# Optimization experiments

Measured on AMD Instinct MI355X. Metric: run time of the kernel, lower is better.

The kernel has to match this reference:

```python
import jax, jax.numpy as jnp
import numpy as np

N_HEADS = 16
ROPE_THETA = 10000.0


def _rope_cos_sin(T, head_dim, dtype):
    # freqs: (head_dim//2,), angles: (T, head_dim//2)
    freqs = 1.0 / ROPE_THETA ** (jnp.arange(0, head_dim, 2, dtype=jnp.float32) / head_dim)
    ang = jnp.arange(T, dtype=jnp.float32)[:, None] * freqs[None, :]
    return jnp.cos(ang).astype(dtype), jnp.sin(ang).astype(dtype)


def _apply_rope(x, cos, sin):
    # x: (B, H, T, D); cos/sin: (T, D//2)
    D = x.shape[-1]
    x1, x2 = x[..., : D // 2], x[..., D // 2 :]
    return jnp.concatenate([x1 * cos - x2 * sin, x1 * sin + x2 * cos], axis=-1)


def setup_inputs() -> dict:
    key = jax.random.key(0)
    ks = jax.random.split(key, 5)
    B, T, C = 2, 2048, 1024
    x = jax.random.normal(ks[0], (B, T, C), dtype=jnp.float32)
    w_attn = jax.random.normal(ks[1], (C, 3 * C), dtype=jnp.float32) * (C ** -0.5)
    b_attn = jax.random.normal(ks[2], (3 * C,), dtype=jnp.float32) * 0.02
    w_proj = jax.random.normal(ks[3], (C, C), dtype=jnp.float32) * (C ** -0.5)
    b_proj = jax.random.normal(ks[4], (C,), dtype=jnp.float32) * 0.02
    return {
        "x": x,
        "w_attn": w_attn,
        "b_attn": b_attn,
        "w_proj": w_proj,
        "b_proj": b_proj,
        "last_k_no_attend": 0,
        "window_size": 0,
    }


def reference(x, w_attn, b_attn, w_proj, b_proj, last_k_no_attend, window_size):
    B, T, C = x.shape
    H = N_HEADS
    D = C // H
    qkv = x @ w_attn + b_attn  # (B, T, 3C)
    q, k, v = jnp.split(qkv, 3, axis=-1)
    # (B, T, C) -> (B, H, T, D)
    to_heads = lambda t: t.reshape(B, T, H, D).transpose(0, 2, 1, 3)
    q, k, v = to_heads(q), to_heads(k), to_heads(v)
    cos, sin = _rope_cos_sin(T, D, x.dtype)
    q = _apply_rope(q, cos, sin)
    k = _apply_rope(k, cos, sin)
    scale = D ** -0.5
    attn = jnp.einsum("bhqd,bhkd->bhqk", q, k) * scale  # (B, H, T, T)
    causal = jnp.tril(jnp.ones((T, T), dtype=bool))
    attn = jnp.where(causal, attn, -jnp.inf)
    # last_k_no_attend/window_size default to 0 -> the custom-mask branch is
    # skipped (the nonzero branch in the source is ill-defined: it zeroes
    # entire rows producing NaN softmax).
    attn = jax.nn.softmax(attn, axis=-1)
    y = jnp.einsum("bhqk,bhkd->bhqd", attn, v)  # (B, H, T, D)
    y = y.transpose(0, 2, 1, 3).reshape(B, T, C)
    return y @ w_proj + b_proj
```

## Files before the change

kernel.cpp:

```cpp
#include <hip/hip_runtime.h>
#include <hip/hip_bf16.h>

typedef __bf16 bf16_t;
typedef __bf16 bf16x8 __attribute__((ext_vector_type(8)));
typedef float f32x4 __attribute__((ext_vector_type(4)));
typedef float f32x8v __attribute__((ext_vector_type(8)));

#define B_    2
#define T_    2048
#define C_    1024
#define H_    16
#define D_    64
#define M_    4096
#define NQKV_ 3072
#define PLD   72
#define NQT2  16
#define GTILE (128 * 64)
#define SLOTE 16384

static __device__ __forceinline__ float  bf2f(bf16_t x) { return (float)x; }
static __device__ __forceinline__ bf16_t f2bf(float x)  { return (bf16_t)x; }

typedef const __attribute__((address_space(1))) void gas_void;
typedef __attribute__((address_space(3))) void las_void;
static __device__ __forceinline__ void gld16(const void* g, void* l) {
  __builtin_amdgcn_global_load_lds((gas_void*)g, (las_void*)l, 16, 0, 0);
}

__global__ __launch_bounds__(256) void rope_tab_k(float2* __restrict__ tab) {
  int i = blockIdx.x * 256 + threadIdx.x;
  int tpos = i >> 5, d = i & 31;
  float fr = exp2f(-(float)d * (13.287712379549449f / 32.0f));
  float ang = (float)tpos * fr;
  tab[i] = make_float2(cosf(ang), sinf(ang));
}

__global__ __launch_bounds__(256) void f32_to_bf16_k(const float* __restrict__ in,
                                                     bf16_t* __restrict__ out) {
  const int i = (blockIdx.x * 256 + threadIdx.x) * 8;
  f32x8v v = *(const f32x8v*)(in + i);
  bf16x8 h;
#pragma unroll
  for (int j = 0; j < 8; ++j) h[j] = f2bf(v[j]);
  *(bf16x8*)(out + i) = h;
}

__global__ __launch_bounds__(256) void transpose_f32_bf16(const float* __restrict__ in,
                                                          bf16_t* __restrict__ out,
                                                          int R, int Ccols) {
  __shared__ bf16_t tile[32][33];
  int tx = threadIdx.x & 31, ty = threadIdx.x >> 5;
  int c0 = blockIdx.x * 32, r0 = blockIdx.y * 32;
#pragma unroll
  for (int j = 0; j < 4; ++j)
    tile[ty + j * 8][tx] = f2bf(in[(size_t)(r0 + ty + j * 8) * Ccols + c0 + tx]);
  __syncthreads();
#pragma unroll
  for (int j = 0; j < 4; ++j)
    out[(size_t)(c0 + ty + j * 8) * R + r0 + tx] = tile[tx][ty + j * 8];
}

__device__ __forceinline__ void gemm_core(const bf16_t* __restrict__ A,
                                          const bf16_t* __restrict__ Bt,
                                          int m0, int n0,
                                          bf16_t* sm,
                                          f32x4 acc[4][4]) {
  const int t    = threadIdx.x;
  const int lane = t & 63, w = t >> 6;
  const int wr = (w >> 1) * 64, wc = (w & 1) * 64;
  const int l15 = lane & 15, g4 = lane >> 4;

  const f32x4 z4 = {0.f, 0.f, 0.f, 0.f};
#pragma unroll
  for (int i = 0; i < 4; ++i)
#pragma unroll
    for (int j = 0; j < 4; ++j) acc[i][j] = z4;

  const int srow = w * 32 + (lane >> 3);
  const int sel8 = (lane & 7) * 8;
  const bf16_t* gA = A  + (size_t)(m0 + srow) * C_ + sel8;
  const bf16_t* gB = Bt + (size_t)(n0 + srow) * C_ + sel8;
  const int dOff = (w * 32) * 64;

#pragma unroll
  for (int j = 0; j < 4; ++j) {
    gld16(gA + (size_t)(j * 8) * C_, sm + dOff + j * 8 * 64);
    gld16(gB + (size_t)(j * 8) * C_, sm + GTILE + dOff + j * 8 * 64);
  }
  __syncthreads();

  int cur = 0;
  for (int kt = 0; kt < C_ / 64; ++kt) {
    if (kt + 1 < C_ / 64) {
      const int k0 = (kt + 1) * 64;
      bf16_t* nA = sm + (cur ^ 1) * (2 * GTILE);
      bf16_t* nB = nA + GTILE;
#pragma unroll
      for (int j = 0; j < 4; ++j) {
        gld16(gA + (size_t)(j * 8) * C_ + k0, nA + dOff + j * 8 * 64);
        gld16(gB + (size_t)(j * 8) * C_ + k0, nB + dOff + j * 8 * 64);
      }
    }
    const bf16_t* lA = sm + cur * (2 * GTILE);
    const bf16_t* lB = lA + GTILE;
#pragma unroll
    for (int ks = 0; ks < 2; ++ks) {
      bf16x8 af[4], bfv[4];
#pragma unroll
      for (int mi = 0; mi < 4; ++mi)
        af[mi] = *(const bf16x8*)&lA[(wr + mi * 16 + l15) * 64 + ks * 32 + g4 * 8];
#pragma unroll
      for (int ni = 0; ni < 4; ++ni)
        bfv[ni] = *(const bf16x8*)&lB[(wc + ni * 16 + l15) * 64 + ks * 32 + g4 * 8];
#pragma unroll
      for (int mi = 0; mi < 4; ++mi)
#pragma unroll
        for (int ni = 0; ni < 4; ++ni)
          acc[mi][ni] = __builtin_amdgcn_mfma_f32_16x16x32_bf16(af[mi], bfv[ni],
                                                                acc[mi][ni], 0, 0, 0);
    }
    __syncthreads();
    cur ^= 1;
  }
}

__global__ __launch_bounds__(512, 2) void qkv_gemm(const bf16_t* __restrict__ x,
                                                   const bf16_t* __restrict__ wT,
                                                   const float* __restrict__ bias,
                                                   const float2* __restrict__ rtab,
                                                   bf16_t* __restrict__ qo,
                                                   bf16_t* __restrict__ ko,
                                                   bf16_t* __restrict__ vo) {
  __shared__ __align__(16) bf16_t sm[4 * SLOTE];
  const int t = threadIdx.x;
  const int lane = t & 63, w = t >> 6;
  const int l15 = lane & 15, g4 = lane >> 4;
  const int wr = (w >> 2) * 128, wc = (w & 3) * 64;

  const int bid = blockIdx.x;
  const int swz = (bid & 7) * 24 + (bid >> 3);
  const int m0 = (swz & 15) * 256, n0 = (swz >> 4) * 256;

  const f32x4 z4 = {0.f, 0.f, 0.f, 0.f};
  f32x4 acc[8][4];
#pragma unroll
  for (int i = 0; i < 8; ++i)
#pragma unroll
    for (int j = 0; j < 4; ++j) acc[i][j] = z4;

  const int sr  = (lane >> 2);
  const int sc8 = (lane & 3) * 8;
  const bf16_t* gA = x  + (size_t)(m0 + w * 32 + sr) * C_ + sc8;
  const bf16_t* gB = wT + (size_t)(n0 + w * 32 + sr) * C_ + sc8;

#define QKV_STAGE(h)                                                            \
  {                                                                             \
    bf16_t* sl = sm + ((h) & 3) * SLOTE;                                        \
    const size_t kofs = (size_t)(h) * 32;                                       \
    gld16(gA + kofs,            sl + (w * 32) * 32);                            \
    gld16(gA + 16 * C_ + kofs,  sl + (w * 32 + 16) * 32);                       \
    gld16(gB + kofs,            sl + 8192 + (w * 32) * 32);                     \
    gld16(gB + 16 * C_ + kofs,  sl + 8192 + (w * 32 + 16) * 32);                \
  }

  QKV_STAGE(0);
  QKV_STAGE(1);

  for (int h = 0; h < 32; ++h) {
    if (h < 31) asm volatile("s_waitcnt vmcnt(4)" ::: "memory");
    else        asm volatile("s_waitcnt vmcnt(0)" ::: "memory");
    __builtin_amdgcn_sched_barrier(0);
    __builtin_amdgcn_s_barrier();
    __builtin_amdgcn_sched_barrier(0);
    if (h + 2 < 32) QKV_STAGE(h + 2);

    const bf16_t* sl = sm + (h & 3) * SLOTE;
    bf16x8 af[8], bfv[4];
#pragma unroll
    for (int mi = 0; mi < 8; ++mi)
      af[mi] = *(const bf16x8*)&sl[(wr + mi * 16 + l15) * 32 + g4 * 8];
#pragma unroll
    for (int ni = 0; ni < 4; ++ni)
      bfv[ni] = *(const bf16x8*)&sl[8192 + (wc + ni * 16 + l15) * 32 + g4 * 8];
#pragma unroll
    for (int mi = 0; mi < 8; ++mi)
#pragma unroll
      for (int ni = 0; ni < 4; ++ni)
        acc[mi][ni] = __builtin_amdgcn_mfma_f32_16x16x32_bf16(af[mi], bfv[ni],
                                                              acc[mi][ni], 0, 0, 0);
  }
#undef QKV_STAGE

  __syncthreads();
  bf16_t* stg = sm + w * 8192;

  const int ng  = n0 + wc;
  const int sel = ng >> 10;
  const int h2  = (ng & 1023) >> 6;

  if (sel < 2) {
    const float qs = (sel == 0) ? 0.125f * 1.4426950408889634f : 1.0f;
#pragma unroll
    for (int mi = 0; mi < 8; ++mi) {
#pragma unroll
      for (int ni = 0; ni < 2; ++ni) {
        const int d1 = ni * 16 + l15;
        const float b1 = bias[ng + d1];
        const float b2 = bias[ng + d1 + 32];
#pragma unroll
        for (int r = 0; r < 4; ++r) {
          const int lrow = mi * 16 + g4 * 4 + r;
          const int tpos = (m0 + wr + lrow) & (T_ - 1);
          const float2 cs = rtab[tpos * 32 + d1];
          const float x1 = acc[mi][ni][r]     + b1;
          const float x2 = acc[mi][ni + 2][r] + b2;
          stg[lrow * 64 + d1]      = f2bf((x1 * cs.x - x2 * cs.y) * qs);
          stg[lrow * 64 + d1 + 32] = f2bf((x1 * cs.y + x2 * cs.x) * qs);
        }
      }
    }
  } else {
#pragma unroll
    for (int mi = 0; mi < 8; ++mi)
#pragma unroll
      for (int ni = 0; ni < 4; ++ni) {
        const int d = ni * 16 + l15;
        const float b1 = bias[ng + d];
#pragma unroll
        for (int r = 0; r < 4; ++r)
          stg[(mi * 16 + g4 * 4 + r) * 64 + d] = f2bf(acc[mi][ni][r] + b1);
      }
  }

  bf16_t* outp = (sel == 0) ? qo : (sel == 1 ? ko : vo);
  const int a  = lane >> 3;
  const int b8 = (lane & 7) * 8;
#pragma unroll
  for (int p = 0; p < 16; ++p) {
    const int lrow = p * 8 + a;
    const int row  = m0 + wr + lrow;
    const int tpos = row & (T_ - 1);
    const int bb   = row >> 11;
    uint4 val = *(const uint4*)&stg[lrow * 64 + b8];
    *(uint4*)(outp + ((size_t)(bb * H_ + h2) * T_ + tpos) * D_ + b8) = val;
  }
}

__global__ __launch_bounds__(512) void attn_fwd(const bf16_t* __restrict__ q,
                                                const bf16_t* __restrict__ k,
                                                const bf16_t* __restrict__ v,
                                                bf16_t* __restrict__ y) {
  __shared__ __align__(16) bf16_t Ks[64 * 64];
  __shared__ __align__(16) bf16_t Vt[64 * PLD];
  const int t = threadIdx.x;
  const int lane = t & 63, w = t >> 6;
  const int l15 = lane & 15, g4 = lane >> 4;

  const int f   = blockIdx.x;
  const int idx = f & 255;
  const int bh  = idx & 31;
  const int p   = idx >> 5;
  const int qt  = (f >> 8) ? (15 - p) : p;
  const int qb  = qt * 128;
  const size_t hb = (size_t)bh * T_ * D_;

  const int qrow = qb + w * 16 + l15;
  bf16x8 qf[2];
  qf[0] = *(const bf16x8*)(q + hb + (size_t)qrow * D_ + g4 * 8);
  qf[1] = *(const bf16x8*)(q + hb + (size_t)qrow * D_ + 32 + g4 * 8);

  const f32x4 z4 = {0.f, 0.f, 0.f, 0.f};
  f32x4 o[4];
#pragma unroll
  for (int i = 0; i < 4; ++i) o[i] = z4;
  float mx = -1e30f, L = 0.f;

  const int skk = t >> 3;
  const int sd0 = (t & 7) * 8;
  const int u   = t & 7;
  const int ksw = sd0 ^ ((skk & 7) * 8);
  const int slot = ((skk >> 5) & 1) * 32 + ((skk >> 2) & 3) * 8 + ((skk >> 4) & 1) * 4 + (skk & 3);
  const int pos  = (((slot >> 3) ^ u) << 3) | (slot & 7);
  const int rowb = qb + w * 16 + g4 * 4;

  const int ntiles = 2 * qt + 2;

  uint4 kv = *(const uint4*)(k + hb + (size_t)skk * D_ + sd0);
  uint4 vv = *(const uint4*)(v + hb + (size_t)skk * D_ + sd0);

  for (int it = 0; it < ntiles; ++it) {
    const int kb = it * 64;
    __syncthreads();
    *(uint4*)&Ks[skk * 64 + ksw] = kv;
    {
      const bf16_t* vb = (const bf16_t*)&vv;
#pragma unroll
      for (int i = 0; i < 8; ++i)
        Vt[(sd0 + i) * PLD + pos] = vb[i];
    }
    __syncthreads();

    if (it + 1 < ntiles) {
      const size_t nb = hb + (size_t)(kb + 64 + skk) * D_ + sd0;
      kv = *(const uint4*)(k + nb);
      vv = *(const uint4*)(v + nb);
    }

    const bool last = (it == ntiles - 1);
    if (last && w < 4) continue;

    f32x4 s[4];
#pragma unroll
    for (int c = 0; c < 4; ++c) s[c] = z4;
#pragma unroll
    for (int ks = 0; ks < 2; ++ks)
#pragma unroll
      for (int c = 0; c < 4; ++c) {
        const int kr = c * 16 + l15;
        bf16x8 kf = *(const bf16x8*)&Ks[kr * 64 + ((ks * 32 + g4 * 8) ^ ((kr & 7) * 8))];
        s[c] = __builtin_amdgcn_mfma_f32_16x16x32_bf16(kf, qf[ks], s[c], 0, 0, 0);
      }

    if (last || (it == ntiles - 2 && w < 4)) {
#pragma unroll
      for (int c = 0; c < 4; ++c)
#pragma unroll
        for (int r = 0; r < 4; ++r)
          if (kb + c * 16 + g4 * 4 + r > qrow) s[c][r] = -1e30f;
    }

    float tm = -1e30f;
#pragma unroll
    for (int c = 0; c < 4; ++c)
#pragma unroll
      for (int r = 0; r < 4; ++r) tm = fmaxf(tm, s[c][r]);
    tm = fmaxf(tm, __shfl_xor(tm, 16));
    tm = fmaxf(tm, __shfl_xor(tm, 32));
    if (!__all(tm - mx <= 8.0f)) {
      const float mnew = fmaxf(mx, tm);
      const float sc = exp2f(mx - mnew);
      L *= sc;
      float scr[4];
#pragma unroll
      for (int r = 0; r < 4; ++r)
        scr[r] = __shfl(sc, (lane & 48) | (g4 * 4 + r));
#pragma unroll
      for (int nf = 0; nf < 4; ++nf)
#pragma unroll
        for (int r = 0; r < 4; ++r) o[nf][r] *= scr[r];
      mx = mnew;
    }
    float rs = 0.f;
#pragma unroll
    for (int c = 0; c < 4; ++c)
#pragma unroll
      for (int r = 0; r < 4; ++r) {
        s[c][r] = exp2f(s[c][r] - mx);
        rs += s[c][r];
      }
    rs += __shfl_xor(rs, 16);
    rs += __shfl_xor(rs, 32);
    L += rs;

    bf16x8 ap0, ap1;
#pragma unroll
    for (int r = 0; r < 4; ++r) {
      ap0[r]     = f2bf(s[0][r]);
      ap0[4 + r] = f2bf(s[1][r]);
      ap1[r]     = f2bf(s[2][r]);
      ap1[4 + r] = f2bf(s[3][r]);
    }

#pragma unroll
    for (int nf = 0; nf < 4; ++nf) {
      const int d  = nf * 16 + l15;
      const int h3 = (2 * nf + (l15 >> 3)) & 7;
      bf16x8 vf0 = *(const bf16x8*)&Vt[d * PLD + ((g4 ^ h3) << 3)];
      bf16x8 vf1 = *(const bf16x8*)&Vt[d * PLD + (((g4 + 4) ^ h3) << 3)];
      o[nf] = __builtin_amdgcn_mfma_f32_16x16x32_bf16(ap0, vf0, o[nf], 0, 0, 0);
      o[nf] = __builtin_amdgcn_mfma_f32_16x16x32_bf16(ap1, vf1, o[nf], 0, 0, 0);
    }
  }

  const int bb = bh / H_, hh = bh % H_;
  float il[4];
#pragma unroll
  for (int r = 0; r < 4; ++r)
    il[r] = 1.0f / __shfl(L, (lane & 48) | (g4 * 4 + r));
#pragma unroll
  for (int nf = 0; nf < 4; ++nf)
#pragma unroll
    for (int r = 0; r < 4; ++r) {
      const int row = rowb + r;
      y[(size_t)(bb * T_ + row) * C_ + hh * D_ + nf * 16 + l15] = f2bf(o[nf][r] * il[r]);
    }
}

__global__ __launch_bounds__(256) void proj_gemm(const bf16_t* __restrict__ yin,
                                                 const bf16_t* __restrict__ wT,
                                                 const float* __restrict__ bias,
                                                 float* __restrict__ out) {
  __shared__ __align__(16) bf16_t smem[4 * GTILE];
  f32x4 acc[4][4];
  const int bid = blockIdx.x;
  const int swz = (bid & 7) * 32 + (bid >> 3);
  const int m0 = (swz & 31) * 128, n0 = (swz >> 5) * 128;
  gemm_core(yin, wT, m0, n0, smem, acc);

  const int t = threadIdx.x;
  const int lane = t & 63, w = t >> 6;
  const int wr = (w >> 1) * 64, wc = (w & 1) * 64;
  const int l15 = lane & 15, g4 = lane >> 4;
  const int ng = n0 + wc;
#pragma unroll
  for (int mi = 0; mi < 4; ++mi) {
    const int rowb = m0 + wr + mi * 16 + g4 * 4;
#pragma unroll
    for (int ni = 0; ni < 4; ++ni) {
      const int n = ng + ni * 16 + l15;
      const float b1 = bias[n];
#pragma unroll
      for (int r = 0; r < 4; ++r)
        out[(size_t)(rowb + r) * C_ + n] = acc[mi][ni][r] + b1;
    }
  }
}

extern "C" void kernel_launch(void* const* d_in, const int* in_sizes, int n_in,
                              void* d_out, int out_size, void* d_ws, size_t ws_size,
                              hipStream_t stream) {
  (void)in_sizes; (void)n_in; (void)out_size; (void)ws_size;
  const float* x      = (const float*)d_in[0];
  const float* w_attn = (const float*)d_in[1];
  const float* b_attn = (const float*)d_in[2];
  const float* w_proj = (const float*)d_in[3];
  const float* b_proj = (const float*)d_in[4];
  float* out = (float*)d_out;

  char* ws = (char*)d_ws;
  bf16_t* wTa = (bf16_t*)ws;  ws += (size_t)NQKV_ * C_ * 2;
  bf16_t* wTp = (bf16_t*)ws;  ws += (size_t)C_ * C_ * 2;
  bf16_t* qb  = (bf16_t*)ws;  ws += (size_t)B_ * H_ * T_ * D_ * 2;
  bf16_t* kb  = (bf16_t*)ws;  ws += (size_t)B_ * H_ * T_ * D_ * 2;
  bf16_t* vb  = (bf16_t*)ws;  ws += (size_t)B_ * H_ * T_ * D_ * 2;
  bf16_t* yb  = (bf16_t*)ws;  ws += (size_t)B_ * T_ * C_ * 2;
  float2* rtab = (float2*)ws; ws += (size_t)T_ * 32 * sizeof(float2);
  bf16_t* x_bf = yb;

  rope_tab_k<<<dim3(T_ * 32 / 256), 256, 0, stream>>>(rtab);
  transpose_f32_bf16<<<dim3(NQKV_ / 32, C_ / 32), 256, 0, stream>>>(w_attn, wTa, C_, NQKV_);
  transpose_f32_bf16<<<dim3(C_ / 32,   C_ / 32), 256, 0, stream>>>(w_proj, wTp, C_, C_);
  f32_to_bf16_k<<<dim3(M_ * C_ / (256 * 8)), 256, 0, stream>>>(x, x_bf);
  qkv_gemm<<<dim3((M_ / 256) * (NQKV_ / 256)), 512, 0, stream>>>(x_bf, wTa, b_attn, rtab, qb, kb, vb);
  attn_fwd<<<dim3(NQT2 * 32), 512, 0, stream>>>(qb, kb, vb, yb);
  proj_gemm<<<dim3((M_ / 128) * (C_ / 128)), 256, 0, stream>>>(yb, wTp, b_proj, out);
}
```

Baseline: 118.3 us.

## Deepen QKV GEMM k-step with XOR swizzle and pair attention q-tiles per block

The QKV GEMM now stages 64-wide k slices into a 2-slot, XOR-swizzled LDS buffer instead of 32-wide slices in 4 slots. This halves the barrier count and aims to reduce LDS bank conflicts, but it gives up the two-deep prefetch because the loop waits on vmcnt(0) every step. The attention kernel now runs 256 blocks, and each block processes a short and a long causal q-tile in sequence. This balances work per block and removes the second wave of launches. MFMA sections are wrapped in s_setprio to favour matrix issue across waves.

```diff
diff --git a/kernel.cpp b/kernel.cpp
--- a/kernel.cpp
+++ b/kernel.cpp
@@ -14,9 +14,8 @@
 #define M_    4096
 #define NQKV_ 3072
 #define PLD   72
-#define NQT2  16
 #define GTILE (128 * 64)
-#define SLOTE 16384
+#define SLOT2 32768
 
 static __device__ __forceinline__ float  bf2f(bf16_t x) { return (float)x; }
 static __device__ __forceinline__ bf16_t f2bf(float x)  { return (bf16_t)x; }
@@ -131,7 +130,7 @@
                                                    bf16_t* __restrict__ qo,
                                                    bf16_t* __restrict__ ko,
                                                    bf16_t* __restrict__ vo) {
-  __shared__ __align__(16) bf16_t sm[4 * SLOTE];
+  __shared__ __align__(16) bf16_t sm[2 * SLOT2];
   const int t = threadIdx.x;
   const int lane = t & 63, w = t >> 6;
   const int l15 = lane & 15, g4 = lane >> 4;
@@ -148,46 +147,55 @@
 #pragma unroll
     for (int j = 0; j < 4; ++j) acc[i][j] = z4;
 
-  const int sr  = (lane >> 2);
-  const int sc8 = (lane & 3) * 8;
-  const bf16_t* gA = x  + (size_t)(m0 + w * 32 + sr) * C_ + sc8;
-  const bf16_t* gB = wT + (size_t)(n0 + w * 32 + sr) * C_ + sc8;
+  const int sr8 = lane >> 3;
+  const int swc = ((lane & 7) ^ ((lane >> 3) & 7)) * 8;
+  const bf16_t* gA = x  + (size_t)(m0 + w * 32 + sr8) * C_ + swc;
+  const bf16_t* gB = wT + (size_t)(n0 + w * 32 + sr8) * C_ + swc;
 
 #define QKV_STAGE(h)                                                            \
   {                                                                             \
-    bf16_t* sl = sm + ((h) & 3) * SLOTE;                                        \
-    const size_t kofs = (size_t)(h) * 32;                                       \
-    gld16(gA + kofs,            sl + (w * 32) * 32);                            \
-    gld16(gA + 16 * C_ + kofs,  sl + (w * 32 + 16) * 32);                       \
-    gld16(gB + kofs,            sl + 8192 + (w * 32) * 32);                     \
-    gld16(gB + 16 * C_ + kofs,  sl + 8192 + (w * 32 + 16) * 32);                \
+    bf16_t* sl = sm + ((h) & 1) * SLOT2;                                        \
+    const size_t kofs = (size_t)(h) * 64;                                       \
+    gld16(gA + kofs,            sl + (w * 32 +  0) * 64);                       \
+    gld16(gA +  8 * C_ + kofs,  sl + (w * 32 +  8) * 64);                       \
+    gld16(gA + 16 * C_ + kofs,  sl + (w * 32 + 16) * 64);                       \
+    gld16(gA + 24 * C_ + kofs,  sl + (w * 32 + 24) * 64);                       \
+    gld16(gB + kofs,            sl + 16384 + (w * 32 +  0) * 64);               \
+    gld16(gB +  8 * C_ + kofs,  sl + 16384 + (w * 32 +  8) * 64);               \
+    gld16(gB + 16 * C_ + kofs,  sl + 16384 + (w * 32 + 16) * 64);               \
+    gld16(gB + 24 * C_ + kofs,  sl + 16384 + (w * 32 + 24) * 64);               \
   }
 
   QKV_STAGE(0);
-  QKV_STAGE(1);
-
-  for (int h = 0; h < 32; ++h) {
-    if (h < 31) asm volatile("s_waitcnt vmcnt(4)" ::: "memory");
-    else        asm volatile("s_waitcnt vmcnt(0)" ::: "memory");
+
+  const int csw = l15 & 7;
+
+  for (int h = 0; h < 16; ++h) {
+    asm volatile("s_waitcnt vmcnt(0)" ::: "memory");
     __builtin_amdgcn_sched_barrier(0);
     __builtin_amdgcn_s_barrier();
     __builtin_amdgcn_sched_barrier(0);
-    if (h + 2 < 32) QKV_STAGE(h + 2);
-
-    const bf16_t* sl = sm + (h & 3) * SLOTE;
-    bf16x8 af[8], bfv[4];
-#pragma unroll
-    for (int mi = 0; mi < 8; ++mi)
-      af[mi] = *(const bf16x8*)&sl[(wr + mi * 16 + l15) * 32 + g4 * 8];
-#pragma unroll
-    for (int ni = 0; ni < 4; ++ni)
-      bfv[ni] = *(const bf16x8*)&sl[8192 + (wc + ni * 16 + l15) * 32 + g4 * 8];
-#pragma unroll
-    for (int mi = 0; mi < 8; ++mi)
+    if (h + 1 < 16) QKV_STAGE(h + 1);
+
+    const bf16_t* sl = sm + (h & 1) * SLOT2;
+#pragma unroll
+    for (int ks = 0; ks < 2; ++ks) {
+      bf16x8 af[8], bfv[4];
+#pragma unroll
+      for (int mi = 0; mi < 8; ++mi)
+        af[mi] = *(const bf16x8*)&sl[(wr + mi * 16 + l15) * 64 + (((ks * 4 + g4) ^ csw) * 8)];
 #pragma unroll
       for (int ni = 0; ni < 4; ++ni)
-        acc[mi][ni] = __builtin_amdgcn_mfma_f32_16x16x32_bf16(af[mi], bfv[ni],
-                                                              acc[mi][ni], 0, 0, 0);
+        bfv[ni] = *(const bf16x8*)&sl[16384 + (wc + ni * 16 + l15) * 64 + (((ks * 4 + g4) ^ csw) * 8)];
+      __builtin_amdgcn_s_setprio(1);
+#pragma unroll
+      for (int mi = 0; mi < 8; ++mi)
+#pragma unroll
+        for (int ni = 0; ni < 4; ++ni)
+          acc[mi][ni] = __builtin_amdgcn_mfma_f32_16x16x32_bf16(af[mi], bfv[ni],
+                                                                acc[mi][ni], 0, 0, 0);
+      __builtin_amdgcn_s_setprio(0);
+    }
   }
 #undef QKV_STAGE
 
@@ -256,24 +264,10 @@
   const int lane = t & 63, w = t >> 6;
   const int l15 = lane & 15, g4 = lane >> 4;
 
-  const int f   = blockIdx.x;
-  const int idx = f & 255;
-  const int bh  = idx & 31;
-  const int p   = idx >> 5;
-  const int qt  = (f >> 8) ? (15 - p) : p;
-  const int qb  = qt * 128;
+  const int f  = blockIdx.x;
+  const int bh = f & 31;
+  const int p  = (f >> 5) & 7;
   const size_t hb = (size_t)bh * T_ * D_;
-
-  const int qrow = qb + w * 16 + l15;
-  bf16x8 qf[2];
-  qf[0] = *(const bf16x8*)(q + hb + (size_t)qrow * D_ + g4 * 8);
-  qf[1] = *(const bf16x8*)(q + hb + (size_t)qrow * D_ + 32 + g4 * 8);
-
-  const f32x4 z4 = {0.f, 0.f, 0.f, 0.f};
-  f32x4 o[4];
-#pragma unroll
-  for (int i = 0; i < 4; ++i) o[i] = z4;
-  float mx = -1e30f, L = 0.f;
 
   const int skk = t >> 3;
   const int sd0 = (t & 7) * 8;
@@ -281,119 +275,141 @@
   const int ksw = sd0 ^ ((skk & 7) * 8);
   const int slot = ((skk >> 5) & 1) * 32 + ((skk >> 2) & 3) * 8 + ((skk >> 4) & 1) * 4 + (skk & 3);
   const int pos  = (((slot >> 3) ^ u) << 3) | (slot & 7);
-  const int rowb = qb + w * 16 + g4 * 4;
-
-  const int ntiles = 2 * qt + 2;
-
-  uint4 kv = *(const uint4*)(k + hb + (size_t)skk * D_ + sd0);
-  uint4 vv = *(const uint4*)(v + hb + (size_t)skk * D_ + sd0);
-
-  for (int it = 0; it < ntiles; ++it) {
-    const int kb = it * 64;
-    __syncthreads();
-    *(uint4*)&Ks[skk * 64 + ksw] = kv;
-    {
-      const bf16_t* vb = (const bf16_t*)&vv;
-#pragma unroll
-      for (int i = 0; i < 8; ++i)
-        Vt[(sd0 + i) * PLD + pos] = vb[i];
-    }
-    __syncthreads();
-
-    if (it + 1 < ntiles) {
-      const size_t nb = hb + (size_t)(kb + 64 + skk) * D_ + sd0;
-      kv = *(const uint4*)(k + nb);
-      vv = *(const uint4*)(v + nb);
-    }
-
-    const bool last = (it == ntiles - 1);
-    if (last && w < 4) continue;
-
-    f32x4 s[4];
-#pragma unroll
-    for (int c = 0; c < 4; ++c) s[c] = z4;
-#pragma unroll
-    for (int ks = 0; ks < 2; ++ks)
-#pragma unroll
-      for (int c = 0; c < 4; ++c) {
-        const int kr = c * 16 + l15;
-        bf16x8 kf = *(const bf16x8*)&Ks[kr * 64 + ((ks * 32 + g4 * 8) ^ ((kr & 7) * 8))];
-        s[c] = __builtin_amdgcn_mfma_f32_16x16x32_bf16(kf, qf[ks], s[c], 0, 0, 0);
-      }
-
-    if (last || (it == ntiles - 2 && w < 4)) {
+  const int bb = bh / H_, hh = bh % H_;
+
+  const f32x4 z4 = {0.f, 0.f, 0.f, 0.f};
+
+#pragma unroll 1
+  for (int half = 0; half < 2; ++half) {
+    const int qt = half ? (15 - p) : p;
+    const int qb = qt * 128;
+    const int qrow = qb + w * 16 + l15;
+    const int rowb = qb + w * 16 + g4 * 4;
+
+    bf16x8 qf[2];
+    qf[0] = *(const bf16x8*)(q + hb + (size_t)qrow * D_ + g4 * 8);
+    qf[1] = *(const bf16x8*)(q + hb + (size_t)qrow * D_ + 32 + g4 * 8);
+
+    f32x4 o[4];
+#pragma unroll
+    for (int i = 0; i < 4; ++i) o[i] = z4;
+    float mx = -1e30f, L = 0.f;
+
+    const int ntiles = 2 * qt + 2;
+
+    uint4 kv = *(const uint4*)(k + hb + (size_t)skk * D_ + sd0);
+    uint4 vv = *(const uint4*)(v + hb + (size_t)skk * D_ + sd0);
+
+    for (int it = 0; it < ntiles; ++it) {
+      const int kb = it * 64;
+      __syncthreads();
+      *(uint4*)&Ks[skk * 64 + ksw] = kv;
+      {
+        const bf16_t* vb = (const bf16_t*)&vv;
+#pragma unroll
+        for (int i = 0; i < 8; ++i)
+          Vt[(sd0 + i) * PLD + pos] = vb[i];
+      }
+      __syncthreads();
+
+      if (it + 1 < ntiles) {
+        const size_t nb = hb + (size_t)(kb + 64 + skk) * D_ + sd0;
+        kv = *(const uint4*)(k + nb);
+        vv = *(const uint4*)(v + nb);
+      }
+
+      const bool last = (it == ntiles - 1);
+      if (last && w < 4) continue;
+
+      f32x4 s[4];
+#pragma unroll
+      for (int c = 0; c < 4; ++c) s[c] = z4;
+      __builtin_amdgcn_s_setprio(1);
+#pragma unroll
+      for (int ks = 0; ks < 2; ++ks)
+#pragma unroll
+        for (int c = 0; c < 4; ++c) {
+          const int kr = c * 16 + l15;
+          bf16x8 kf = *(const bf16x8*)&Ks[kr * 64 + ((ks * 32 + g4 * 8) ^ ((kr & 7) * 8))];
+          s[c] = __builtin_amdgcn_mfma_f32_16x16x32_bf16(kf, qf[ks], s[c], 0, 0, 0);
+        }
+      __builtin_amdgcn_s_setprio(0);
+
+      if (last || (it == ntiles - 2 && w < 4)) {
+#pragma unroll
+        for (int c = 0; c < 4; ++c)
+#pragma unroll
+          for (int r = 0; r < 4; ++r)
+            if (kb + c * 16 + g4 * 4 + r > qrow) s[c][r] = -1e30f;
+      }
+
+      float tm = -1e30f;
 #pragma unroll
       for (int c = 0; c < 4; ++c)
 #pragma unroll
+        for (int r = 0; r < 4; ++r) tm = fmaxf(tm, s[c][r]);
+      tm = fmaxf(tm, __shfl_xor(tm, 16));
+      tm = fmaxf(tm, __shfl_xor(tm, 32));
+      if (!__all(tm - mx <= 8.0f)) {
+        const float mnew = fmaxf(mx, tm);
+        const float sc = exp2f(mx - mnew);
+        L *= sc;
+        float scr[4];
+#pragma unroll
         for (int r = 0; r < 4; ++r)
-          if (kb + c * 16 + g4 * 4 + r > qrow) s[c][r] = -1e30f;
-    }
-
-    float tm = -1e30f;
-#pragma unroll
-    for (int c = 0; c < 4; ++c)
-#pragma unroll
-      for (int r = 0; r < 4; ++r) tm = fmaxf(tm, s[c][r]);
-    tm = fmaxf(tm, __shfl_xor(tm, 16));
-    tm = fmaxf(tm, __shfl_xor(tm, 32));
-    if (!__all(tm - mx <= 8.0f)) {
-      const float mnew = fmaxf(mx, tm);
-      const float sc = exp2f(mx - mnew);
-      L *= sc;
-      float scr[4];
-#pragma unroll
-      for (int r = 0; r < 4; ++r)
-        scr[r] = __shfl(sc, (lane & 48) | (g4 * 4 + r));
-#pragma unroll
-      for (int nf = 0; nf < 4; ++nf)
-#pragma unroll
-        for (int r = 0; r < 4; ++r) o[nf][r] *= scr[r];
-      mx = mnew;
-    }
-    float rs = 0.f;
-#pragma unroll
-    for (int c = 0; c < 4; ++c)
+          scr[r] = __shfl(sc, (lane & 48) | (g4 * 4 + r));
+#pragma unroll
+        for (int nf = 0; nf < 4; ++nf)
+#pragma unroll
+          for (int r = 0; r < 4; ++r) o[nf][r] *= scr[r];
+        mx = mnew;
+      }
+      float rs = 0.f;
+#pragma unroll
+      for (int c = 0; c < 4; ++c)
+#pragma unroll
+        for (int r = 0; r < 4; ++r) {
+          s[c][r] = exp2f(s[c][r] - mx);
+          rs += s[c][r];
+        }
+      rs += __shfl_xor(rs, 16);
+      rs += __shfl_xor(rs, 32);
+      L += rs;
+
+      bf16x8 ap0, ap1;
 #pragma unroll
       for (int r = 0; r < 4; ++r) {
-        s[c][r] = exp2f(s[c][r] - mx);
-        rs += s[c][r];
-      }
-    rs += __shfl_xor(rs, 16);
-    rs += __shfl_xor(rs, 32);
-    L += rs;
-
-    bf16x8 ap0, ap1;
-#pragma unroll
-    for (int r = 0; r < 4; ++r) {
-      ap0[r]     = f2bf(s[0][r]);
-      ap0[4 + r] = f2bf(s[1][r]);
-      ap1[r]     = f2bf(s[2][r]);
-      ap1[4 + r] = f2bf(s[3][r]);
-    }
-
-#pragma unroll
-    for (int nf = 0; nf < 4; ++nf) {
-      const int d  = nf * 16 + l15;
-      const int h3 = (2 * nf + (l15 >> 3)) & 7;
-      bf16x8 vf0 = *(const bf16x8*)&Vt[d * PLD + ((g4 ^ h3) << 3)];
-      bf16x8 vf1 = *(const bf16x8*)&Vt[d * PLD + (((g4 + 4) ^ h3) << 3)];
-      o[nf] = __builtin_amdgcn_mfma_f32_16x16x32_bf16(ap0, vf0, o[nf], 0, 0, 0);
-      o[nf] = __builtin_amdgcn_mfma_f32_16x16x32_bf16(ap1, vf1, o[nf], 0, 0, 0);
-    }
-  }
-
-  const int bb = bh / H_, hh = bh % H_;
-  float il[4];
-#pragma unroll
-  for (int r = 0; r < 4; ++r)
-    il[r] = 1.0f / __shfl(L, (lane & 48) | (g4 * 4 + r));
-#pragma unroll
-  for (int nf = 0; nf < 4; ++nf)
-#pragma unroll
-    for (int r = 0; r < 4; ++r) {
-      const int row = rowb + r;
-      y[(size_t)(bb * T_ + row) * C_ + hh * D_ + nf * 16 + l15] = f2bf(o[nf][r] * il[r]);
-    }
+        ap0[r]     = f2bf(s[0][r]);
+        ap0[4 + r] = f2bf(s[1][r]);
+        ap1[r]     = f2bf(s[2][r]);
+        ap1[4 + r] = f2bf(s[3][r]);
+      }
+
+      __builtin_amdgcn_s_setprio(1);
+#pragma unroll
+      for (int nf = 0; nf < 4; ++nf) {
+        const int d  = nf * 16 + l15;
+        const int h3 = (2 * nf + (l15 >> 3)) & 7;
+        bf16x8 vf0 = *(const bf16x8*)&Vt[d * PLD + ((g4 ^ h3) << 3)];
+        bf16x8 vf1 = *(const bf16x8*)&Vt[d * PLD + (((g4 + 4) ^ h3) << 3)];
+        o[nf] = __builtin_amdgcn_mfma_f32_16x16x32_bf16(ap0, vf0, o[nf], 0, 0, 0);
+        o[nf] = __builtin_amdgcn_mfma_f32_16x16x32_bf16(ap1, vf1, o[nf], 0, 0, 0);
+      }
+      __builtin_amdgcn_s_setprio(0);
+    }
+
+    float il[4];
+#pragma unroll
+    for (int r = 0; r < 4; ++r)
+      il[r] = 1.0f / __shfl(L, (lane & 48) | (g4 * 4 + r));
+#pragma unroll
+    for (int nf = 0; nf < 4; ++nf)
+#pragma unroll
+      for (int r = 0; r < 4; ++r) {
+        const int row = rowb + r;
+        y[(size_t)(bb * T_ + row) * C_ + hh * D_ + nf * 16 + l15] = f2bf(o[nf][r] * il[r]);
+      }
+  }
 }
 
 __global__ __launch_bounds__(256) void proj_gemm(const bf16_t* __restrict__ yin,
@@ -452,6 +468,6 @@
   transpose_f32_bf16<<<dim3(C_ / 32,   C_ / 32), 256, 0, stream>>>(w_proj, wTp, C_, C_);
   f32_to_bf16_k<<<dim3(M_ * C_ / (256 * 8)), 256, 0, stream>>>(x, x_bf);
   qkv_gemm<<<dim3((M_ / 256) * (NQKV_ / 256)), 512, 0, stream>>>(x_bf, wTa, b_attn, rtab, qb, kb, vb);
-  attn_fwd<<<dim3(NQT2 * 32), 512, 0, stream>>>(qb, kb, vb, yb);
+  attn_fwd<<<dim3(256), 512, 0, stream>>>(qb, kb, vb, yb);
   proj_gemm<<<dim3((M_ / 128) * (C_ / 128)), 256, 0, stream>>>(yb, wTp, b_proj, out);
 }
```

New measurement: 117.4 us. Within noise of the previous version (-0.8%).
